# Optimization experiments

Measured on AMD Instinct MI355X. Metric: run time of the kernel, lower is better.

## Reference

```python
import jax, jax.numpy as jnp
import numpy as np

EMBED_DIM = 1024
NUM_HEADS = 16
HEAD_DIM = EMBED_DIM // NUM_HEADS
# Source divides by scale = head_dim**-0.5, i.e. multiplies logits by sqrt(head_dim).
INV_SCALE = float(HEAD_DIM) ** 0.5


def setup_inputs() -> dict:
    key = jax.random.key(0)
    ks = jax.random.split(key, 9)
    E = EMBED_DIM
    s = 1.0 / np.sqrt(E)
    x = jax.random.normal(ks[0], (2, 2048, E), dtype=jnp.float32)
    Wq = jax.random.uniform(ks[1], (E, E), jnp.float32, -s, s)
    bq = jax.random.uniform(ks[2], (E,), jnp.float32, -s, s)
    Wk = jax.random.uniform(ks[3], (E, E), jnp.float32, -s, s)
    bk = jax.random.uniform(ks[4], (E,), jnp.float32, -s, s)
    Wv = jax.random.uniform(ks[5], (E, E), jnp.float32, -s, s)
    bv = jax.random.uniform(ks[6], (E,), jnp.float32, -s, s)
    Wo = jax.random.uniform(ks[7], (E, E), jnp.float32, -s, s)
    bo = jax.random.uniform(ks[8], (E,), jnp.float32, -s, s)
    return {"x": x, "Wq": Wq, "bq": bq, "Wk": Wk, "bk": bk,
            "Wv": Wv, "bv": bv, "Wo": Wo, "bo": bo}


def reference(x, Wq, bq, Wk, bk, Wv, bv, Wo, bo):
    B, N, C = x.shape
    H, D = NUM_HEADS, HEAD_DIM
    # nn.Linear: y = x @ W.T + b
    q = (x @ Wq.T + bq).reshape(B, N, H, D).transpose(0, 2, 1, 3)  # [B,H,N,D]
    k = (x @ Wk.T + bk).reshape(B, N, H, D).transpose(0, 2, 1, 3)
    v = (x @ Wv.T + bv).reshape(B, N, H, D).transpose(0, 2, 1, 3)
    # Faithful to source: logits = QK^T / (head_dim**-0.5) = QK^T * sqrt(head_dim)
    logits = jnp.einsum('bhnd,bhmd->bhnm', q, k) * INV_SCALE  # [B,H,N,N]
    attn = jax.nn.softmax(logits, axis=-1)
    h = jnp.einsum('bhnm,bhmd->bhnd', attn, v)  # [B,H,N,D]
    concat_h = h.transpose(0, 2, 1, 3).reshape(B, N, C)
    return concat_h @ Wo.T + bo
```

## Files before the change

kernel.cpp:

```cpp
#include <hip/hip_runtime.h>
#include <math.h>

#define B_ 2
#define N_ 2048
#define E_ 1024
#define H_ 16
#define D_ 64

typedef unsigned short US;
typedef _Float16 h16x8 __attribute__((ext_vector_type(8)));
typedef __fp16 fp16x2 __attribute__((ext_vector_type(2)));
typedef float f32x4 __attribute__((ext_vector_type(4)));
#define MFMA16F(a,b,c) __builtin_amdgcn_mfma_f32_16x16x32_f16(a,b,c,0,0,0)
#define SCL  11.5415603828f

union HU { _Float16 h; US u; };
__device__ __forceinline__ US f2h(float f){ HU x; x.h = (_Float16)f; return x.u; }
__device__ __forceinline__ unsigned pkrtz(float a, float b){
  union { fp16x2 h; unsigned u; } x;
  x.h = __builtin_amdgcn_cvt_pkrtz(a, b);
  return x.u;
}

union U8 { US u[8]; uint4 v; };
union U4 { US u[4]; uint2 v; };

__device__ __forceinline__ void glds16(const US* g, US* l){
  __builtin_amdgcn_global_load_lds(
    (const __attribute__((address_space(1))) unsigned int*)(const void*)g,
    (__attribute__((address_space(3))) unsigned int*)(void*)l, 16, 0, 0);
}

__global__ __launch_bounds__(256) void conv_all(
    const float* __restrict__ x,
    const float* __restrict__ w0, const float* __restrict__ w1,
    const float* __restrict__ w2, const float* __restrict__ w3,
    US* __restrict__ xh, US* __restrict__ Wall)
{
  const int id = blockIdx.x;
  const float* s; US* d; size_t off;
  if (id < 2048) { s = x; d = xh; off = (size_t)id*2048; }
  else {
    int j = id - 2048, wsel = j>>9;
    off = (size_t)(j&511)*2048;
    s = (wsel==0)?w0:(wsel==1)?w1:(wsel==2)?w2:w3;
    d = Wall + (size_t)wsel*1048576;
  }
  size_t i = off + (size_t)threadIdx.x*8;
  float f[8];
  *(float4*)&f[0] = *(const float4*)&s[i];
  *(float4*)&f[4] = *(const float4*)&s[i+4];
  U8 h;
  #pragma unroll
  for (int j=0;j<8;++j) h.u[j] = f2h(f[j]);
  *(uint4*)&d[i] = h.v;
}

__global__ __launch_bounds__(256,2) void qkv_gemm(
    const US* __restrict__ A, const US* __restrict__ Wall,
    const float* __restrict__ bq, const float* __restrict__ bk, const float* __restrict__ bv,
    US* __restrict__ Qf, US* __restrict__ Kf, US* __restrict__ Vtb)
{
  __shared__ __align__(16) US sA[128*32];
  __shared__ __align__(16) US sW[192*32];
  const int t = threadIdx.x;
  const int w = t>>6, lane = t&63;
  const int q = lane>>4, c = lane&15;
  const int gm0 = blockIdx.y*128, gn0 = blockIdx.x*64;
  const int r16 = lane>>2, seg = lane&3;

  f32x4 acc[3][2][4] = {};
  for (int kb = 0; kb < 1024; kb += 32) {
    glds16(&A[(size_t)(gm0 + w*32      + r16)*1024 + kb + seg*8], &sA[(w*32)*32]);
    glds16(&A[(size_t)(gm0 + w*32 + 16 + r16)*1024 + kb + seg*8], &sA[(w*32+16)*32]);
    #pragma unroll
    for (int p=0;p<3;++p){
      int cw = w*3 + p;
      int z = cw>>2, r0 = (cw&3)*16;
      glds16(&Wall[(size_t)z*1048576 + (size_t)(gn0 + r0 + r16)*1024 + kb + seg*8],
             &sW[(z*64 + r0)*32]);
    }
    __syncthreads();
    h16x8 af0 = *(const h16x8*)&sA[(w*32+c)*32 + q*8];
    h16x8 af1 = *(const h16x8*)&sA[(w*32+16+c)*32 + q*8];
    #pragma unroll
    for (int z=0; z<3; ++z)
      #pragma unroll
      for (int ct=0; ct<4; ++ct){
        h16x8 wf = *(const h16x8*)&sW[(z*64+ct*16+c)*32 + q*8];
        acc[z][0][ct] = MFMA16F(af0, wf, acc[z][0][ct]);
        acc[z][1][ct] = MFMA16F(af1, wf, acc[z][1][ct]);
      }
    __syncthreads();
  }
  #pragma unroll
  for (int z=0; z<3; ++z)
  #pragma unroll
  for (int rt=0; rt<2; ++rt)
  #pragma unroll
  for (int ct=0; ct<4; ++ct) {
    int col = gn0 + ct*16 + c;
    float bv_ = (z==0 ? bq : z==1 ? bk : bv)[col];
    int rowb = gm0 + w*32 + rt*16 + q*4;
    int hh = col>>6, d = col & 63;
    if (z==2) {
      int b = rowb>>11, n = rowb & (N_-1);
      U4 pk;
      #pragma unroll
      for (int r=0;r<4;++r) pk.u[r] = f2h(acc[z][rt][ct][r] + bv_);
      *(uint2*)&Vtb[((size_t)(b*H_+hh)*D_ + d)*N_ + n] = pk.v;
    } else {
      US* dst = (z==0) ? Qf : Kf;
      #pragma unroll
      for (int r=0;r<4;++r) {
        int row = rowb + r;
        float v = acc[z][rt][ct][r] + bv_;
        if (z==0) v *= SCL;
        int b = row>>11, n = row & (N_-1);
        dst[((size_t)(b*H_+hh)*N_+n)*D_ + d] = f2h(v);
      }
    }
  }
}

__global__ __launch_bounds__(256,4) void o_gemm(
    const US* __restrict__ A, const US* __restrict__ W,
    const float* __restrict__ bias, float* __restrict__ out)
{
  __shared__ __align__(16) US sA[128*32];
  __shared__ __align__(16) US sW[64*32];
  const int t = threadIdx.x;
  const int w = t>>6, lane = t&63;
  const int q = lane>>4, c = lane&15;
  const int gm0 = blockIdx.y*128, gn0 = blockIdx.x*64;
  const int r16 = lane>>2, seg = lane&3;

  f32x4 acc[2][4] = {};
  for (int kb = 0; kb < 1024; kb += 32) {
    glds16(&A[(size_t)(gm0 + w*32      + r16)*1024 + kb + seg*8], &sA[(w*32)*32]);
    glds16(&A[(size_t)(gm0 + w*32 + 16 + r16)*1024 + kb + seg*8], &sA[(w*32+16)*32]);
    glds16(&W[(size_t)(gn0 + w*16      + r16)*1024 + kb + seg*8], &sW[(w*16)*32]);
    __syncthreads();
    h16x8 af0 = *(const h16x8*)&sA[(w*32+c)*32 + q*8];
    h16x8 af1 = *(const h16x8*)&sA[(w*32+16+c)*32 + q*8];
    #pragma unroll
    for (int ct=0; ct<4; ++ct){
      h16x8 wf = *(const h16x8*)&sW[(ct*16+c)*32 + q*8];
      acc[0][ct] = MFMA16F(af0, wf, acc[0][ct]);
      acc[1][ct] = MFMA16F(af1, wf, acc[1][ct]);
    }
    __syncthreads();
  }
  #pragma unroll
  for (int rt=0; rt<2; ++rt)
  #pragma unroll
  for (int ct=0; ct<4; ++ct) {
    int col = gn0 + ct*16 + c;
    float bv_ = bias[col];
    int rowb = gm0 + w*32 + rt*16 + q*4;
    #pragma unroll
    for (int r=0;r<4;++r)
      out[(size_t)(rowb+r)*1024 + col] = acc[rt][ct][r] + bv_;
  }
}

#define KSTR2 72
#define VSTR  136
__global__ __launch_bounds__(256,2) void attn(
    const US* __restrict__ Qf, const US* __restrict__ Kf, const US* __restrict__ Vt,
    US* __restrict__ Hout)
{
  __shared__ __align__(16) US sK [128*KSTR2];
  __shared__ __align__(16) US sVt[64*VSTR];
  __shared__ __align__(16) US sP [4][16*VSTR];
  const int t = threadIdx.x;
  const int w = t>>6, lane = t&63, q = lane>>4, c = lane&15;
  const int id = blockIdx.x;
  const int bh = ((id & 7) << 2) | ((id >> 3) & 3);
  const int n0 = (id >> 5) * 128;
  const US* Kp = Kf + (size_t)bh * (N_*D_);
  const US* Vp = Vt + (size_t)bh * (D_*N_);

  h16x8 qb[2][2];
  #pragma unroll
  for (int g=0; g<2; ++g){
    const size_t qoff = (size_t)bh*(N_*D_) + (size_t)(n0 + w*32 + g*16 + c)*D_;
    qb[g][0] = *(const h16x8*)&Qf[qoff + q*8];
    qb[g][1] = *(const h16x8*)&Qf[qoff + 32 + q*8];
  }
  h16x8 vones;
  #pragma unroll
  for (int j=0;j<8;++j) vones[j] = (_Float16)1.0f;

  float mi[2] = {-INFINITY, -INFINITY};
  f32x4 o[2][5] = {};

  const int kr = t>>3, kc8 = (t&7)*8;
  const int vr = t>>4, vc8 = (t&15)*8;

  for (int mt=0; mt<16; ++mt) {
    const int m0 = mt*128;
    #pragma unroll
    for (int p=0;p<4;++p){
      int r = p*32 + kr;
      *(uint4*)&sK[r*KSTR2 + kc8] = *(const uint4*)&Kp[(size_t)(m0 + r)*D_ + kc8];
    }
    #pragma unroll
    for (int p=0;p<4;++p){
      int r = p*16 + vr;
      *(uint4*)&sVt[r*VSTR + vc8] = *(const uint4*)&Vp[(size_t)r*N_ + m0 + vc8];
    }
    __syncthreads();

    f32x4 s[2][8];
    #pragma unroll
    for (int f=0; f<8; ++f){
      h16x8 k0 = *(const h16x8*)&sK[(f*16+c)*KSTR2 + q*8];
      h16x8 k1 = *(const h16x8*)&sK[(f*16+c)*KSTR2 + 32 + q*8];
      #pragma unroll
      for (int g=0; g<2; ++g){
        f32x4 sv = {};
        sv = MFMA16F(k0, qb[g][0], sv);
        sv = MFMA16F(k1, qb[g][1], sv);
        s[g][f] = sv;
      }
    }

    h16x8 pa[2][4];
    #pragma unroll
    for (int g=0; g<2; ++g){
      f32x4 vm = s[g][0];
      #pragma unroll
      for (int f=1; f<8; ++f){
        vm[0]=fmaxf(vm[0],s[g][f][0]); vm[1]=fmaxf(vm[1],s[g][f][1]);
        vm[2]=fmaxf(vm[2],s[g][f][2]); vm[3]=fmaxf(vm[3],s[g][f][3]);
      }
      float v = fmaxf(fmaxf(vm[0],vm[1]), fmaxf(vm[2],vm[3]));
      v = fmaxf(v, __shfl_xor(v, 16));
      v = fmaxf(v, __shfl_xor(v, 32));
      float mnew = fmaxf(mi[g], v);
      if (!__all(v <= mi[g])) {
        float alpha = exp2f(mi[g]-mnew);
        float ar[4];
        #pragma unroll
        for (int r=0; r<4; ++r) ar[r] = __shfl(alpha, q*4+r);
        #pragma unroll
        for (int dt=0; dt<5; ++dt){
          o[g][dt][0]*=ar[0]; o[g][dt][1]*=ar[1]; o[g][dt][2]*=ar[2]; o[g][dt][3]*=ar[3];
        }
      }
      mi[g] = mnew;
      #pragma unroll
      for (int f=0; f<8; ++f){
        float p0 = exp2f(s[g][f][0]-mnew);
        float p1 = exp2f(s[g][f][1]-mnew);
        float p2 = exp2f(s[g][f][2]-mnew);
        float p3 = exp2f(s[g][f][3]-mnew);
        uint2 pk;
        pk.x = pkrtz(p0, p1);
        pk.y = pkrtz(p2, p3);
        *(uint2*)&sP[w][c*VSTR + f*16 + q*4] = pk;
      }
      #pragma unroll
      for (int kc=0; kc<4; ++kc)
        pa[g][kc] = *(const h16x8*)&sP[w][c*VSTR + kc*32 + q*8];
    }

    #pragma unroll
    for (int dt=0; dt<4; ++dt){
      h16x8 vf[4];
      #pragma unroll
      for (int kc=0; kc<4; ++kc)
        vf[kc] = *(const h16x8*)&sVt[(dt*16+c)*VSTR + kc*32 + q*8];
      #pragma unroll
      for (int g=0; g<2; ++g)
        #pragma unroll
        for (int kc=0; kc<4; ++kc)
          o[g][dt] = MFMA16F(pa[g][kc], vf[kc], o[g][dt]);
    }
    #pragma unroll
    for (int g=0; g<2; ++g)
      #pragma unroll
      for (int kc=0; kc<4; ++kc)
        o[g][4] = MFMA16F(pa[g][kc], vones, o[g][4]);
    __syncthreads();
  }

  const int b = bh>>4, hh = bh&15;
  #pragma unroll
  for (int g=0; g<2; ++g){
    float ir[4];
    #pragma unroll
    for (int r=0; r<4; ++r) ir[r] = 1.0f / o[g][4][r];
    #pragma unroll
    for (int dt=0; dt<4; ++dt){
      #pragma unroll
      for (int r=0; r<4; ++r){
        int n = n0 + w*32 + g*16 + q*4 + r;
        int d = dt*16 + c;
        Hout[((size_t)(b*N_+n)*H_+hh)*D_ + d] = f2h(o[g][dt][r] * ir[r]);
      }
    }
  }
}

extern "C" void kernel_launch(void* const* d_in, const int* in_sizes, int n_in,
                              void* d_out, int out_size, void* d_ws, size_t ws_size,
                              hipStream_t stream)
{
  const float* x  = (const float*)d_in[0];
  const float* Wq = (const float*)d_in[1];
  const float* bq = (const float*)d_in[2];
  const float* Wk = (const float*)d_in[3];
  const float* bk = (const float*)d_in[4];
  const float* Wv = (const float*)d_in[5];
  const float* bv = (const float*)d_in[6];
  const float* Wo = (const float*)d_in[7];
  const float* bo = (const float*)d_in[8];
  US* ws  = (US*)d_ws;
  const size_t M1 = 1048576;
  US* xh   = ws;
  US* Wall = ws + 4*M1;
  US* Qf   = ws + 8*M1;
  US* Kf   = ws + 12*M1;
  US* Vtb  = ws + 16*M1;
  US* Hf   = ws + 20*M1;

  conv_all<<<4096, 256, 0, stream>>>(x, Wq, Wk, Wv, Wo, xh, Wall);
  qkv_gemm<<<dim3(16,32), 256, 0, stream>>>(xh, Wall, bq, bk, bv, Qf, Kf, Vtb);
  attn<<<512, 256, 0, stream>>>(Qf, Kf, Vtb, Hf);
  o_gemm<<<dim3(16,32), 256, 0, stream>>>(Hf, Wall + 3*M1, bo, (float*)d_out);
}
```

Measured before the change: 213.9 us.

## Retile QKV GEMM per projection and use 8-wave attention blocks

The QKV GEMM now launches one grid slice per projection (blockIdx.z) with 128x128 tiles, each wave computing a 64x64 sub-tile, in place of one block covering all three projections at 128x64. The attention kernel moves from 256 to 512 threads per block, so each wave handles 16 query rows instead of 32. This lowers per-wave register pressure and raises the wave count on the attention kernel. In exchange each K/V tile loaded to shared memory is reused across fewer rows per wave, and there are more LDS reads per MFMA.

```diff
diff --git a/kernel.cpp b/kernel.cpp
--- a/kernel.cpp
+++ b/kernel.cpp
@@ -56,65 +56,65 @@
   *(uint4*)&d[i] = h.v;
 }
 
-__global__ __launch_bounds__(256,2) void qkv_gemm(
+__global__ __launch_bounds__(256,3) void qkv_gemm(
     const US* __restrict__ A, const US* __restrict__ Wall,
     const float* __restrict__ bq, const float* __restrict__ bk, const float* __restrict__ bv,
     US* __restrict__ Qf, US* __restrict__ Kf, US* __restrict__ Vtb)
 {
   __shared__ __align__(16) US sA[128*32];
-  __shared__ __align__(16) US sW[192*32];
+  __shared__ __align__(16) US sW[128*32];
+  const int z = blockIdx.z;
+  const US* W = Wall + (size_t)z*1048576;
+  const float* bias = (z==0)?bq:(z==1)?bk:bv;
+
   const int t = threadIdx.x;
   const int w = t>>6, lane = t&63;
   const int q = lane>>4, c = lane&15;
-  const int gm0 = blockIdx.y*128, gn0 = blockIdx.x*64;
+  const int mq = (w>>1)*64, nq = (w&1)*64;
+  const int gm0 = blockIdx.y*128, gn0 = blockIdx.x*128;
   const int r16 = lane>>2, seg = lane&3;
 
-  f32x4 acc[3][2][4] = {};
+  f32x4 acc[4][4] = {};
   for (int kb = 0; kb < 1024; kb += 32) {
-    glds16(&A[(size_t)(gm0 + w*32      + r16)*1024 + kb + seg*8], &sA[(w*32)*32]);
-    glds16(&A[(size_t)(gm0 + w*32 + 16 + r16)*1024 + kb + seg*8], &sA[(w*32+16)*32]);
-    #pragma unroll
-    for (int p=0;p<3;++p){
-      int cw = w*3 + p;
-      int z = cw>>2, r0 = (cw&3)*16;
-      glds16(&Wall[(size_t)z*1048576 + (size_t)(gn0 + r0 + r16)*1024 + kb + seg*8],
-             &sW[(z*64 + r0)*32]);
-    }
-    __syncthreads();
-    h16x8 af0 = *(const h16x8*)&sA[(w*32+c)*32 + q*8];
-    h16x8 af1 = *(const h16x8*)&sA[(w*32+16+c)*32 + q*8];
-    #pragma unroll
-    for (int z=0; z<3; ++z)
-      #pragma unroll
-      for (int ct=0; ct<4; ++ct){
-        h16x8 wf = *(const h16x8*)&sW[(z*64+ct*16+c)*32 + q*8];
-        acc[z][0][ct] = MFMA16F(af0, wf, acc[z][0][ct]);
-        acc[z][1][ct] = MFMA16F(af1, wf, acc[z][1][ct]);
-      }
-    __syncthreads();
-  }
-  #pragma unroll
-  for (int z=0; z<3; ++z)
-  #pragma unroll
-  for (int rt=0; rt<2; ++rt)
-  #pragma unroll
-  for (int ct=0; ct<4; ++ct) {
-    int col = gn0 + ct*16 + c;
-    float bv_ = (z==0 ? bq : z==1 ? bk : bv)[col];
-    int rowb = gm0 + w*32 + rt*16 + q*4;
+    #pragma unroll
+    for (int p=0;p<2;++p){
+      int rb = (w*2+p)*16;
+      glds16(&A[(size_t)(gm0 + rb + r16)*1024 + kb + seg*8], &sA[rb*32]);
+      glds16(&W[(size_t)(gn0 + rb + r16)*1024 + kb + seg*8], &sW[rb*32]);
+    }
+    __syncthreads();
+    h16x8 af[4], wf[4];
+    #pragma unroll
+    for (int rt=0;rt<4;++rt) af[rt] = *(const h16x8*)&sA[(mq+rt*16+c)*32 + q*8];
+    #pragma unroll
+    for (int ct=0;ct<4;++ct) wf[ct] = *(const h16x8*)&sW[(nq+ct*16+c)*32 + q*8];
+    #pragma unroll
+    for (int rt=0;rt<4;++rt)
+      #pragma unroll
+      for (int ct=0;ct<4;++ct)
+        acc[rt][ct] = MFMA16F(af[rt], wf[ct], acc[rt][ct]);
+    __syncthreads();
+  }
+  #pragma unroll
+  for (int rt=0;rt<4;++rt)
+  #pragma unroll
+  for (int ct=0;ct<4;++ct) {
+    int col = gn0 + nq + ct*16 + c;
+    float bv_ = bias[col];
+    int rowb = gm0 + mq + rt*16 + q*4;
     int hh = col>>6, d = col & 63;
     if (z==2) {
       int b = rowb>>11, n = rowb & (N_-1);
       U4 pk;
       #pragma unroll
-      for (int r=0;r<4;++r) pk.u[r] = f2h(acc[z][rt][ct][r] + bv_);
+      for (int r=0;r<4;++r) pk.u[r] = f2h(acc[rt][ct][r] + bv_);
       *(uint2*)&Vtb[((size_t)(b*H_+hh)*D_ + d)*N_ + n] = pk.v;
     } else {
       US* dst = (z==0) ? Qf : Kf;
       #pragma unroll
       for (int r=0;r<4;++r) {
         int row = rowb + r;
-        float v = acc[z][rt][ct][r] + bv_;
+        float v = acc[rt][ct][r] + bv_;
         if (z==0) v *= SCL;
         int b = row>>11, n = row & (N_-1);
         dst[((size_t)(b*H_+hh)*N_+n)*D_ + d] = f2h(v);
@@ -166,13 +166,13 @@
 
 #define KSTR2 72
 #define VSTR  136
-__global__ __launch_bounds__(256,2) void attn(
+__global__ __launch_bounds__(512,4) void attn(
     const US* __restrict__ Qf, const US* __restrict__ Kf, const US* __restrict__ Vt,
     US* __restrict__ Hout)
 {
   __shared__ __align__(16) US sK [128*KSTR2];
   __shared__ __align__(16) US sVt[64*VSTR];
-  __shared__ __align__(16) US sP [4][16*VSTR];
+  __shared__ __align__(16) US sP [8][16*VSTR];
   const int t = threadIdx.x;
   const int w = t>>6, lane = t&63, q = lane>>4, c = lane&15;
   const int id = blockIdx.x;
@@ -181,19 +181,15 @@
   const US* Kp = Kf + (size_t)bh * (N_*D_);
   const US* Vp = Vt + (size_t)bh * (D_*N_);
 
-  h16x8 qb[2][2];
-  #pragma unroll
-  for (int g=0; g<2; ++g){
-    const size_t qoff = (size_t)bh*(N_*D_) + (size_t)(n0 + w*32 + g*16 + c)*D_;
-    qb[g][0] = *(const h16x8*)&Qf[qoff + q*8];
-    qb[g][1] = *(const h16x8*)&Qf[qoff + 32 + q*8];
-  }
+  const size_t qoff = (size_t)bh*(N_*D_) + (size_t)(n0 + w*16 + c)*D_;
+  h16x8 qb0 = *(const h16x8*)&Qf[qoff + q*8];
+  h16x8 qb1 = *(const h16x8*)&Qf[qoff + 32 + q*8];
   h16x8 vones;
   #pragma unroll
   for (int j=0;j<8;++j) vones[j] = (_Float16)1.0f;
 
-  float mi[2] = {-INFINITY, -INFINITY};
-  f32x4 o[2][5] = {};
+  float mi = -INFINITY;
+  f32x4 o[5] = {};
 
   const int kr = t>>3, kc8 = (t&7)*8;
   const int vr = t>>4, vc8 = (t&15)*8;
@@ -201,105 +197,90 @@
   for (int mt=0; mt<16; ++mt) {
     const int m0 = mt*128;
     #pragma unroll
-    for (int p=0;p<4;++p){
-      int r = p*32 + kr;
+    for (int p=0;p<2;++p){
+      int r = p*64 + kr;
       *(uint4*)&sK[r*KSTR2 + kc8] = *(const uint4*)&Kp[(size_t)(m0 + r)*D_ + kc8];
     }
     #pragma unroll
-    for (int p=0;p<4;++p){
-      int r = p*16 + vr;
+    for (int p=0;p<2;++p){
+      int r = p*32 + vr;
       *(uint4*)&sVt[r*VSTR + vc8] = *(const uint4*)&Vp[(size_t)r*N_ + m0 + vc8];
     }
     __syncthreads();
 
-    f32x4 s[2][8];
+    f32x4 s[8];
     #pragma unroll
     for (int f=0; f<8; ++f){
       h16x8 k0 = *(const h16x8*)&sK[(f*16+c)*KSTR2 + q*8];
       h16x8 k1 = *(const h16x8*)&sK[(f*16+c)*KSTR2 + 32 + q*8];
-      #pragma unroll
-      for (int g=0; g<2; ++g){
-        f32x4 sv = {};
-        sv = MFMA16F(k0, qb[g][0], sv);
-        sv = MFMA16F(k1, qb[g][1], sv);
-        s[g][f] = sv;
+      f32x4 sv = {};
+      sv = MFMA16F(k0, qb0, sv);
+      sv = MFMA16F(k1, qb1, sv);
+      s[f] = sv;
+    }
+
+    f32x4 vm = s[0];
+    #pragma unroll
+    for (int f=1; f<8; ++f){
+      vm[0]=fmaxf(vm[0],s[f][0]); vm[1]=fmaxf(vm[1],s[f][1]);
+      vm[2]=fmaxf(vm[2],s[f][2]); vm[3]=fmaxf(vm[3],s[f][3]);
+    }
+    float v = fmaxf(fmaxf(vm[0],vm[1]), fmaxf(vm[2],vm[3]));
+    v = fmaxf(v, __shfl_xor(v, 16));
+    v = fmaxf(v, __shfl_xor(v, 32));
+    float mnew = fmaxf(mi, v);
+    if (!__all(v <= mi)) {
+      float alpha = exp2f(mi-mnew);
+      float ar[4];
+      #pragma unroll
+      for (int r=0; r<4; ++r) ar[r] = __shfl(alpha, q*4+r);
+      #pragma unroll
+      for (int dt=0; dt<5; ++dt){
+        o[dt][0]*=ar[0]; o[dt][1]*=ar[1]; o[dt][2]*=ar[2]; o[dt][3]*=ar[3];
       }
     }
-
-    h16x8 pa[2][4];
-    #pragma unroll
-    for (int g=0; g<2; ++g){
-      f32x4 vm = s[g][0];
-      #pragma unroll
-      for (int f=1; f<8; ++f){
-        vm[0]=fmaxf(vm[0],s[g][f][0]); vm[1]=fmaxf(vm[1],s[g][f][1]);
-        vm[2]=fmaxf(vm[2],s[g][f][2]); vm[3]=fmaxf(vm[3],s[g][f][3]);
+    mi = mnew;
+    #pragma unroll
+    for (int f=0; f<8; ++f){
+      float p0 = exp2f(s[f][0]-mnew);
+      float p1 = exp2f(s[f][1]-mnew);
+      float p2 = exp2f(s[f][2]-mnew);
+      float p3 = exp2f(s[f][3]-mnew);
+      uint2 pk;
+      pk.x = pkrtz(p0, p1);
+      pk.y = pkrtz(p2, p3);
+      *(uint2*)&sP[w][c*VSTR + f*16 + q*4] = pk;
+    }
+    h16x8 pa[4];
+    #pragma unroll
+    for (int kc=0; kc<4; ++kc)
+      pa[kc] = *(const h16x8*)&sP[w][c*VSTR + kc*32 + q*8];
+
+    #pragma unroll
+    for (int dt=0; dt<4; ++dt){
+      #pragma unroll
+      for (int kc=0; kc<4; ++kc){
+        h16x8 vf = *(const h16x8*)&sVt[(dt*16+c)*VSTR + kc*32 + q*8];
+        o[dt] = MFMA16F(pa[kc], vf, o[dt]);
       }
-      float v = fmaxf(fmaxf(vm[0],vm[1]), fmaxf(vm[2],vm[3]));
-      v = fmaxf(v, __shfl_xor(v, 16));
-      v = fmaxf(v, __shfl_xor(v, 32));
-      float mnew = fmaxf(mi[g], v);
-      if (!__all(v <= mi[g])) {
-        float alpha = exp2f(mi[g]-mnew);
-        float ar[4];
-        #pragma unroll
-        for (int r=0; r<4; ++r) ar[r] = __shfl(alpha, q*4+r);
-        #pragma unroll
-        for (int dt=0; dt<5; ++dt){
-          o[g][dt][0]*=ar[0]; o[g][dt][1]*=ar[1]; o[g][dt][2]*=ar[2]; o[g][dt][3]*=ar[3];
-        }
-      }
-      mi[g] = mnew;
-      #pragma unroll
-      for (int f=0; f<8; ++f){
-        float p0 = exp2f(s[g][f][0]-mnew);
-        float p1 = exp2f(s[g][f][1]-mnew);
-        float p2 = exp2f(s[g][f][2]-mnew);
-        float p3 = exp2f(s[g][f][3]-mnew);
-        uint2 pk;
-        pk.x = pkrtz(p0, p1);
-        pk.y = pkrtz(p2, p3);
-        *(uint2*)&sP[w][c*VSTR + f*16 + q*4] = pk;
-      }
-      #pragma unroll
-      for (int kc=0; kc<4; ++kc)
-        pa[g][kc] = *(const h16x8*)&sP[w][c*VSTR + kc*32 + q*8];
-    }
-
-    #pragma unroll
-    for (int dt=0; dt<4; ++dt){
-      h16x8 vf[4];
-      #pragma unroll
-      for (int kc=0; kc<4; ++kc)
-        vf[kc] = *(const h16x8*)&sVt[(dt*16+c)*VSTR + kc*32 + q*8];
-      #pragma unroll
-      for (int g=0; g<2; ++g)
-        #pragma unroll
-        for (int kc=0; kc<4; ++kc)
-          o[g][dt] = MFMA16F(pa[g][kc], vf[kc], o[g][dt]);
-    }
-    #pragma unroll
-    for (int g=0; g<2; ++g)
-      #pragma unroll
-      for (int kc=0; kc<4; ++kc)
-        o[g][4] = MFMA16F(pa[g][kc], vones, o[g][4]);
+    }
+    #pragma unroll
+    for (int kc=0; kc<4; ++kc)
+      o[4] = MFMA16F(pa[kc], vones, o[4]);
     __syncthreads();
   }
 
   const int b = bh>>4, hh = bh&15;
-  #pragma unroll
-  for (int g=0; g<2; ++g){
-    float ir[4];
-    #pragma unroll
-    for (int r=0; r<4; ++r) ir[r] = 1.0f / o[g][4][r];
-    #pragma unroll
-    for (int dt=0; dt<4; ++dt){
-      #pragma unroll
-      for (int r=0; r<4; ++r){
-        int n = n0 + w*32 + g*16 + q*4 + r;
-        int d = dt*16 + c;
-        Hout[((size_t)(b*N_+n)*H_+hh)*D_ + d] = f2h(o[g][dt][r] * ir[r]);
-      }
+  float ir[4];
+  #pragma unroll
+  for (int r=0; r<4; ++r) ir[r] = 1.0f / o[4][r];
+  #pragma unroll
+  for (int dt=0; dt<4; ++dt){
+    #pragma unroll
+    for (int r=0; r<4; ++r){
+      int n = n0 + w*16 + q*4 + r;
+      int d = dt*16 + c;
+      Hout[((size_t)(b*N_+n)*H_+hh)*D_ + d] = f2h(o[dt][r] * ir[r]);
     }
   }
 }
@@ -327,7 +308,7 @@
   US* Hf   = ws + 20*M1;
 
   conv_all<<<4096, 256, 0, stream>>>(x, Wq, Wk, Wv, Wo, xh, Wall);
-  qkv_gemm<<<dim3(16,32), 256, 0, stream>>>(xh, Wall, bq, bk, bv, Qf, Kf, Vtb);
-  attn<<<512, 256, 0, stream>>>(Qf, Kf, Vtb, Hf);
+  qkv_gemm<<<dim3(8,32,3), 256, 0, stream>>>(xh, Wall, bq, bk, bv, Qf, Kf, Vtb);
+  attn<<<512, 512, 0, stream>>>(Qf, Kf, Vtb, Hf);
   o_gemm<<<dim3(16,32), 256, 0, stream>>>(Hf, Wall + 3*M1, bo, (float*)d_out);
 }
```

Measured after the change: 208.7 us. 2.4% less time.
